# Performance work log

Hardware: AMD Instinct MI355X
Metric: run time of the kernel (lower is better)

Reference implementation:

```python
import jax, jax.numpy as jnp
import numpy as np

BN_EPS = 1e-5


def lstm_scan(x, Wih, Whh, b):
    # x: [B, T, I] -> outputs [B, T, H]; PyTorch gate order i, f, g, o
    B = x.shape[0]
    H = Whh.shape[1]
    xs = jnp.swapaxes(x, 0, 1)  # [T, B, I]

    def step(carry, xt):
        h, c = carry
        z = xt @ Wih.T + h @ Whh.T + b  # [B, 4H]
        i, f, g, o = jnp.split(z, 4, axis=-1)
        c = jax.nn.sigmoid(f) * c + jax.nn.sigmoid(i) * jnp.tanh(g)
        h = jax.nn.sigmoid(o) * jnp.tanh(c)
        return (h, c), h

    init = (jnp.zeros((B, H), x.dtype), jnp.zeros((B, H), x.dtype))
    _, hs = jax.lax.scan(step, init, xs)
    return jnp.swapaxes(hs, 0, 1)


def bilstm(x, Wf, Uf, bf, Wr, Ur, br):
    fwd = lstm_scan(x, Wf, Uf, bf)
    rev = lstm_scan(x[:, ::-1], Wr, Ur, br)[:, ::-1]
    return jnp.concatenate([fwd, rev], axis=-1)


def batchnorm(x, g, b):
    # training-mode BN: batch mean, biased variance (PyTorch forward default)
    mu = x.mean(axis=0)
    var = x.var(axis=0)
    return g * (x - mu) * jax.lax.rsqrt(var + BN_EPS) + b


def setup_inputs() -> dict:
    key = jax.random.key(0)
    ks = jax.random.split(key, 20)
    B = 1048576
    idx = jax.random.randint(ks[0], (B, 1), 0, 8).astype(jnp.float32)
    feats = jax.random.normal(ks[1], (B, 7), dtype=jnp.float32)
    x = jnp.concatenate([idx, feats], axis=1)  # [B, 8]

    def p(k, shape):
        return 0.1 * jax.random.normal(k, shape, dtype=jnp.float32)

    return {
        "x": x,
        "emb": p(ks[2], (8, 2)),
        "W1": p(ks[3], (18, 9)), "b1": p(ks[4], (18,)),
        "g1": jnp.ones((18,), jnp.float32), "be1": jnp.zeros((18,), jnp.float32),
        "W2": p(ks[5], (9, 18)), "b2": p(ks[6], (9,)),
        "g2": jnp.ones((9,), jnp.float32), "be2": jnp.zeros((9,), jnp.float32),
        # lstm1: input 1, hidden 2, bidirectional
        "l1Wf": p(ks[7], (8, 1)), "l1Uf": p(ks[8], (8, 2)), "l1bf": p(ks[9], (8,)),
        "l1Wr": p(ks[10], (8, 1)), "l1Ur": p(ks[11], (8, 2)), "l1br": p(ks[12], (8,)),
        # lstm2: input 4, hidden 1, bidirectional
        "l2Wf": p(ks[13], (4, 4)), "l2Uf": p(ks[14], (4, 1)), "l2bf": p(ks[15], (4,)),
        "l2Wr": p(ks[16], (4, 4)), "l2Ur": p(ks[17], (4, 1)), "l2br": p(ks[18], (4,)),
    }


def reference(x, emb, W1, b1, g1, be1, W2, b2, g2, be2,
              l1Wf, l1Uf, l1bf, l1Wr, l1Ur, l1br,
              l2Wf, l2Uf, l2bf, l2Wr, l2Ur, l2br):
    idx = x[:, 0].astype(jnp.int32)
    e = emb[idx]                                   # [B, 2]
    h = jnp.concatenate([e, x[:, 1:]], axis=1)     # [B, 9]
    h = jax.nn.relu(batchnorm(h @ W1.T + b1, g1, be1))   # [B, 18]
    h = jax.nn.relu(batchnorm(h @ W2.T + b2, g2, be2))   # [B, 9]
    h = h[:, :, None]                              # [B, 9, 1]
    h = jax.nn.relu(bilstm(h, l1Wf, l1Uf, l1bf, l1Wr, l1Ur, l1br))  # [B, 9, 4]
    h = bilstm(h, l2Wf, l2Uf, l2bf, l2Wr, l2Ur, l2br)               # [B, 9, 2]
    return h.reshape(-1, 9, 2)
```

## Files before the change

kernel.cpp:

```cpp
#include <hip/hip_runtime.h>

#define LOG2E 1.4426950408889634f
#define BN_EPS 1e-5f

typedef float f32x2 __attribute__((ext_vector_type(2)));
typedef float f32x4 __attribute__((ext_vector_type(4)));

__device__ __forceinline__ float sigf(float x){
    return __builtin_amdgcn_rcpf(1.f + __builtin_amdgcn_exp2f(-LOG2E * x));
}
__device__ __forceinline__ float sigtanh(float a, float b){
    float A  = __builtin_amdgcn_exp2f(LOG2E * a);
    float Bv = __builtin_amdgcn_exp2f((2.f * LOG2E) * b);
    float num = A * (Bv - 1.f);
    float den = (1.f + A) * (1.f + Bv);
    return num * __builtin_amdgcn_rcpf(den);
}
__device__ __forceinline__ float relu_(float x){ return fmaxf(x, 0.f); }

__device__ __forceinline__ float wsum(float v){
    #pragma unroll
    for (int m = 32; m >= 1; m >>= 1) v += __shfl_xor(v, m, 64);
    return v;
}

__device__ constexpr int TRI(int j, int l){ return j*9 - j*(j-1)/2 + (l - j); }

__device__ __forceinline__ void load_h0(const float* __restrict__ x, const float* __restrict__ emb,
                                        long row, float h0[9])
{
    const float4* xv = (const float4*)(x + row * 8);
    float4 p = xv[0];
    float4 q = xv[1];
    int idx = (int)p.x;
    float2 e = ((const float2*)emb)[idx];
    h0[0] = e.x; h0[1] = e.y;
    h0[2] = p.y; h0[3] = p.z; h0[4] = p.w;
    h0[5] = q.x; h0[6] = q.y; h0[7] = q.z; h0[8] = q.w;
}

__global__ __launch_bounds__(256) void k_moments(const float* __restrict__ x, const float* __restrict__ emb,
                                                 float* __restrict__ stats, int B)
{
    float s9[9], mt[45];
    #pragma unroll
    for (int j = 0; j < 9; ++j) s9[j] = 0.f;
    #pragma unroll
    for (int t = 0; t < 45; ++t) mt[t] = 0.f;

    long base = (long)blockIdx.x * 1024 + threadIdx.x;
    #pragma unroll
    for (int r = 0; r < 4; ++r){
        long row = base + r * 256;
        if (row < B){
            float h0[9];
            load_h0(x, emb, row, h0);
            #pragma unroll
            for (int j = 0; j < 9; ++j){
                s9[j] += h0[j];
                #pragma unroll
                for (int l = j; l < 9; ++l)
                    mt[TRI(j,l)] = fmaf(h0[j], h0[l], mt[TRI(j,l)]);
            }
        }
    }
    __shared__ float sm[54];
    if (threadIdx.x < 54) sm[threadIdx.x] = 0.f;
    __syncthreads();
    bool l0 = (threadIdx.x & 63) == 0;
    #pragma unroll
    for (int j = 0; j < 9; ++j){
        float v = wsum(s9[j]);
        if (l0) atomicAdd(&sm[j], v);
    }
    #pragma unroll
    for (int t = 0; t < 45; ++t){
        float v = wsum(mt[t]);
        if (l0) atomicAdd(&sm[9 + t], v);
    }
    __syncthreads();
    if (threadIdx.x < 9)  atomicAdd(&stats[threadIdx.x], sm[threadIdx.x]);
    else if (threadIdx.x < 54) atomicAdd(&stats[16 + threadIdx.x - 9], sm[threadIdx.x]);
}

__device__ __forceinline__ void bn1_from_moments(const float* __restrict__ stats,
                                                 const float* __restrict__ W1, const float* __restrict__ b1,
                                                 const float* __restrict__ g1, const float* __restrict__ be1,
                                                 float invB, float* smem_sc, float* smem_sh)
{
    if (threadIdx.x < 18){
        int k = threadIdx.x;
        float w[9];
        #pragma unroll
        for (int j = 0; j < 9; ++j) w[j] = W1[k*9 + j];
        float dot9 = 0.f, q = 0.f;
        #pragma unroll
        for (int j = 0; j < 9; ++j){
            dot9 = fmaf(w[j], stats[j], dot9);
            q = fmaf(w[j]*w[j], stats[16 + TRI(j,j)], q);
            #pragma unroll
            for (int l = j+1; l < 9; ++l)
                q = fmaf(2.f*w[j]*w[l], stats[16 + TRI(j,l)], q);
        }
        float m1  = dot9 * invB;
        float var = fmaf(-m1, m1, q * invB);
        float mu  = m1 + b1[k];
        float sc  = g1[k] * __builtin_amdgcn_rsqf(var + BN_EPS);
        smem_sc[k] = sc;
        smem_sh[k] = fmaf(-mu, sc, be1[k]);
    }
    __syncthreads();
}

template<int STORE_Z2>
__global__ __launch_bounds__(256) void k_stats2(const float* __restrict__ x, const float* __restrict__ emb,
                                                const float* __restrict__ W1, const float* __restrict__ b1,
                                                const float* __restrict__ g1, const float* __restrict__ be1,
                                                const float* __restrict__ W2, const float* __restrict__ b2,
                                                float* __restrict__ stats, float* __restrict__ z2buf, int B)
{
    __shared__ float s_sc[18], s_sh[18];
    bn1_from_moments(stats, W1, b1, g1, be1, 1.f/(float)B, s_sc, s_sh);

    float sc1[18], sh1[18];
    #pragma unroll
    for (int k = 0; k < 18; ++k){ sc1[k] = s_sc[k]; sh1[k] = s_sh[k]; }

    float as[9], aq[9];
    #pragma unroll
    for (int k = 0; k < 9; ++k){ as[k] = 0.f; aq[k] = 0.f; }

    long base = (long)blockIdx.x * 1024 + threadIdx.x;
    #pragma unroll
    for (int r = 0; r < 4; ++r){
        long row = base + r * 256;
        if (row < B){
            float h0[9];
            load_h0(x, emb, row, h0);
            float a1[18];
            #pragma unroll
            for (int k = 0; k < 18; ++k){
                float s = b1[k];
                #pragma unroll
                for (int j = 0; j < 9; ++j) s = fmaf(W1[k*9 + j], h0[j], s);
                a1[k] = relu_(fmaf(sc1[k], s, sh1[k]));
            }
            #pragma unroll
            for (int k = 0; k < 9; ++k){
                float s = b2[k];
                #pragma unroll
                for (int j = 0; j < 18; ++j) s = fmaf(W2[k*18 + j], a1[j], s);
                as[k] += s; aq[k] = fmaf(s, s, aq[k]);
                if (STORE_Z2) z2buf[(long)k * B + row] = s;
            }
        }
    }
    __shared__ float sm[18];
    if (threadIdx.x < 18) sm[threadIdx.x] = 0.f;
    __syncthreads();
    bool l0 = (threadIdx.x & 63) == 0;
    #pragma unroll
    for (int k = 0; k < 9; ++k){
        float s = wsum(as[k]);
        float q = wsum(aq[k]);
        if (l0){ atomicAdd(&sm[k], s); atomicAdd(&sm[9 + k], q); }
    }
    __syncthreads();
    if (threadIdx.x < 9)       atomicAdd(&stats[64 + threadIdx.x], sm[threadIdx.x]);
    else if (threadIdx.x < 18) atomicAdd(&stats[80 + threadIdx.x - 9], sm[threadIdx.x]);
}

__device__ __forceinline__ f32x2 mk2(float a, float b){ f32x2 r; r.x=a; r.y=b; return r; }
__device__ __forceinline__ f32x4 mk4(float a, float b, float c, float d){ f32x4 r; r.x=a; r.y=b; r.z=c; r.w=d; return r; }

template<int USE_WS>
__global__ __launch_bounds__(256) void k_main(const float* __restrict__ x, const float* __restrict__ emb,
    const float* __restrict__ W1, const float* __restrict__ b1,
    const float* __restrict__ g1, const float* __restrict__ be1,
    const float* __restrict__ W2, const float* __restrict__ b2,
    const float* __restrict__ g2, const float* __restrict__ be2,
    const float* __restrict__ w1f, const float* __restrict__ u1f, const float* __restrict__ c1f,
    const float* __restrict__ w1r, const float* __restrict__ u1r, const float* __restrict__ c1r,
    const float* __restrict__ w2f, const float* __restrict__ u2f, const float* __restrict__ c2f,
    const float* __restrict__ w2r, const float* __restrict__ u2r, const float* __restrict__ c2r,
    const float* __restrict__ stats, const float* __restrict__ z2buf,
    float* __restrict__ out, int B)
{
    __shared__ float s_sc[18], s_sh[18];
    float invB = 1.f / (float)B;
    if (!USE_WS) bn1_from_moments(stats, W1, b1, g1, be1, invB, s_sc, s_sh);

    long row = (long)blockIdx.x * 256 + threadIdx.x;
    if (row >= B) return;

    float a2[9];
    #pragma unroll
    for (int k = 0; k < 9; ++k){
        float zc;
        if (USE_WS){
            zc = z2buf[(long)k * B + row];
        } else {
            zc = 0.f;
        }
        a2[k] = zc;
    }
    if (!USE_WS){
        float h0[9];
        load_h0(x, emb, row, h0);
        float a1[18];
        #pragma unroll
        for (int k = 0; k < 18; ++k){
            float s = b1[k];
            #pragma unroll
            for (int j = 0; j < 9; ++j) s = fmaf(W1[k*9 + j], h0[j], s);
            a1[k] = relu_(fmaf(s_sc[k], s, s_sh[k]));
        }
        #pragma unroll
        for (int k = 0; k < 9; ++k){
            float s = b2[k];
            #pragma unroll
            for (int j = 0; j < 18; ++j) s = fmaf(W2[k*18 + j], a1[j], s);
            a2[k] = s;
        }
    }
    #pragma unroll
    for (int k = 0; k < 9; ++k){
        float mu  = stats[64 + k] * invB;
        float var = fmaf(-mu, mu, stats[80 + k] * invB);
        float sc  = g2[k] * __builtin_amdgcn_rsqf(var + BN_EPS);
        a2[k] = relu_(fmaf(sc, a2[k] - mu, be2[k]));
    }

    f32x4 W4[4], U04[4], U14[4], B4[4];
    #pragma unroll
    for (int g = 0; g < 4; ++g){
        W4[g]  = mk4(w1f[2*g], w1f[2*g+1], w1r[2*g], w1r[2*g+1]);
        U04[g] = mk4(u1f[(2*g)*2], u1f[(2*g+1)*2], u1r[(2*g)*2], u1r[(2*g+1)*2]);
        U14[g] = mk4(u1f[(2*g)*2+1], u1f[(2*g+1)*2+1], u1r[(2*g)*2+1], u1r[(2*g+1)*2+1]);
        B4[g]  = mk4(c1f[2*g], c1f[2*g+1], c1r[2*g], c1r[2*g+1]);
    }
    f32x4 h4 = {0.f, 0.f, 0.f, 0.f};
    f32x4 c4 = {0.f, 0.f, 0.f, 0.f};
    float u_[9][4];
    #pragma unroll
    for (int s = 0; s < 9; ++s){
        const int tf = s, tr = 8 - s;
        f32x4 xt4 = mk4(a2[tf], a2[tf], a2[tr], a2[tr]);
        f32x4 hx  = mk4(h4.x, h4.x, h4.z, h4.z);
        f32x4 hy  = mk4(h4.y, h4.y, h4.w, h4.w);
        f32x4 z[4];
        #pragma unroll
        for (int g = 0; g < 4; ++g)
            z[g] = __builtin_elementwise_fma(W4[g], xt4,
                    __builtin_elementwise_fma(U04[g], hx,
                     __builtin_elementwise_fma(U14[g], hy, B4[g])));
        f32x4 icg, fs;
        #pragma unroll
        for (int c = 0; c < 4; ++c){
            icg[c] = sigtanh(z[0][c], z[2][c]);
            fs[c]  = sigf(z[1][c]);
        }
        c4 = __builtin_elementwise_fma(fs, c4, icg);
        #pragma unroll
        for (int c = 0; c < 4; ++c) h4[c] = sigtanh(z[3][c], c4[c]);
        u_[tf][0] = relu_(h4.x);
        u_[tf][1] = relu_(h4.y);
        u_[tr][2] = relu_(h4.z);
        u_[tr][3] = relu_(h4.w);
    }

    f32x2 w2v[4][4], u2v[4], b2v[4];
    #pragma unroll
    for (int r = 0; r < 4; ++r){
        #pragma unroll
        for (int j = 0; j < 4; ++j) w2v[r][j] = mk2(w2f[4*r + j], w2r[4*r + j]);
        u2v[r] = mk2(u2f[r], u2r[r]);
        b2v[r] = mk2(c2f[r], c2r[r]);
    }
    f32x2 h2 = {0.f, 0.f};
    f32x2 cc = {0.f, 0.f};
    long obase = row * 18;
    #pragma unroll
    for (int s = 0; s < 9; ++s){
        const int tf = s, tr = 8 - s;
        f32x2 z[4];
        #pragma unroll
        for (int r = 0; r < 4; ++r){
            f32x2 acc = __builtin_elementwise_fma(u2v[r], h2, b2v[r]);
            #pragma unroll
            for (int j = 0; j < 4; ++j)
                acc = __builtin_elementwise_fma(w2v[r][j], mk2(u_[tf][j], u_[tr][j]), acc);
            z[r] = acc;
        }
        f32x2 icg, fs;
        #pragma unroll
        for (int c = 0; c < 2; ++c){
            icg[c] = sigtanh(z[0][c], z[2][c]);
            fs[c]  = sigf(z[1][c]);
        }
        cc = __builtin_elementwise_fma(fs, cc, icg);
        float hfo = sigtanh(z[3][0], cc.x);
        float hro = sigtanh(z[3][1], cc.y);
        h2 = mk2(hfo, hro);
        out[obase + 2*tf]     = hfo;
        out[obase + 2*tr + 1] = hro;
    }
}

extern "C" void kernel_launch(void* const* d_in, const int* in_sizes, int n_in,
                              void* d_out, int out_size, void* d_ws, size_t ws_size,
                              hipStream_t stream)
{
    const float* x    = (const float*)d_in[0];
    const float* emb  = (const float*)d_in[1];
    const float* W1   = (const float*)d_in[2];
    const float* b1   = (const float*)d_in[3];
    const float* g1   = (const float*)d_in[4];
    const float* be1  = (const float*)d_in[5];
    const float* W2   = (const float*)d_in[6];
    const float* b2   = (const float*)d_in[7];
    const float* g2   = (const float*)d_in[8];
    const float* be2  = (const float*)d_in[9];
    const float* l1Wf = (const float*)d_in[10];
    const float* l1Uf = (const float*)d_in[11];
    const float* l1bf = (const float*)d_in[12];
    const float* l1Wr = (const float*)d_in[13];
    const float* l1Ur = (const float*)d_in[14];
    const float* l1br = (const float*)d_in[15];
    const float* l2Wf = (const float*)d_in[16];
    const float* l2Uf = (const float*)d_in[17];
    const float* l2bf = (const float*)d_in[18];
    const float* l2Wr = (const float*)d_in[19];
    const float* l2Ur = (const float*)d_in[20];
    const float* l2br = (const float*)d_in[21];

    int B = in_sizes[0] / 8;
    float* stats = (float*)d_ws;
    float* z2buf = (float*)d_ws + 1024;
    size_t need = (1024 + (size_t)9 * B) * sizeof(float);
    bool use_ws = ws_size >= need;

    hipMemsetAsync(d_ws, 0, 128 * sizeof(float), stream);

    int nb12 = (B + 1023) / 1024;
    int nb3  = (B + 255) / 256;

    k_moments<<<nb12, 256, 0, stream>>>(x, emb, stats, B);
    if (use_ws){
        k_stats2<1><<<nb12, 256, 0, stream>>>(x, emb, W1, b1, g1, be1, W2, b2, stats, z2buf, B);
        k_main<1><<<nb3, 256, 0, stream>>>(x, emb, W1, b1, g1, be1, W2, b2, g2, be2,
                                           l1Wf, l1Uf, l1bf, l1Wr, l1Ur, l1br,
                                           l2Wf, l2Uf, l2bf, l2Wr, l2Ur, l2br,
                                           stats, z2buf, (float*)d_out, B);
    } else {
        k_stats2<0><<<nb12, 256, 0, stream>>>(x, emb, W1, b1, g1, be1, W2, b2, stats, z2buf, B);
        k_main<0><<<nb3, 256, 0, stream>>>(x, emb, W1, b1, g1, be1, W2, b2, g2, be2,
                                           l1Wf, l1Uf, l1bf, l1Wr, l1Ur, l1br,
                                           l2Wf, l2Uf, l2bf, l2Wr, l2Ur, l2br,
                                           stats, z2buf, (float*)d_out, B);
    }
}
```

Baseline: 152.9 us.

## Fuse moment and BN2 stat passes with grid barrier, add prep kernel, persistent grids

```diff
diff --git a/kernel.cpp b/kernel.cpp
--- a/kernel.cpp
+++ b/kernel.cpp
@@ -3,19 +3,15 @@
 #define LOG2E 1.4426950408889634f
 #define BN_EPS 1e-5f
 
-typedef float f32x2 __attribute__((ext_vector_type(2)));
-typedef float f32x4 __attribute__((ext_vector_type(4)));
-
-__device__ __forceinline__ float sigf(float x){
-    return __builtin_amdgcn_rcpf(1.f + __builtin_amdgcn_exp2f(-LOG2E * x));
-}
-__device__ __forceinline__ float sigtanh(float a, float b){
-    float A  = __builtin_amdgcn_exp2f(LOG2E * a);
-    float Bv = __builtin_amdgcn_exp2f((2.f * LOG2E) * b);
-    float num = A * (Bv - 1.f);
-    float den = (1.f + A) * (1.f + Bv);
-    return num * __builtin_amdgcn_rcpf(den);
-}
+#define WS_BAR   120
+#define WS_L1    128
+#define WS_L2    192
+#define WS_BN2S  240
+#define WS_BN2H  249
+#define WS_BN1S  258
+#define WS_BN1H  276
+#define WS_Z2    1024
+
 __device__ __forceinline__ float relu_(float x){ return fmaxf(x, 0.f); }
 
 __device__ __forceinline__ float wsum(float v){
@@ -25,6 +21,10 @@
 }
 
 __device__ constexpr int TRI(int j, int l){ return j*9 - j*(j-1)/2 + (l - j); }
+
+__device__ __forceinline__ float ld_stat(const float* p){
+    return __hip_atomic_load(p, __ATOMIC_RELAXED, __HIP_MEMORY_SCOPE_AGENT);
+}
 
 __device__ __forceinline__ void load_h0(const float* __restrict__ x, const float* __restrict__ emb,
                                         long row, float h0[9])
@@ -39,271 +39,327 @@
     h0[5] = q.x; h0[6] = q.y; h0[7] = q.z; h0[8] = q.w;
 }
 
-__global__ __launch_bounds__(256) void k_moments(const float* __restrict__ x, const float* __restrict__ emb,
-                                                 float* __restrict__ stats, int B)
-{
-    float s9[9], mt[45];
-    #pragma unroll
-    for (int j = 0; j < 9; ++j) s9[j] = 0.f;
-    #pragma unroll
-    for (int t = 0; t < 45; ++t) mt[t] = 0.f;
-
-    long base = (long)blockIdx.x * 1024 + threadIdx.x;
-    #pragma unroll
-    for (int r = 0; r < 4; ++r){
-        long row = base + r * 256;
-        if (row < B){
-            float h0[9];
-            load_h0(x, emb, row, h0);
-            #pragma unroll
-            for (int j = 0; j < 9; ++j){
-                s9[j] += h0[j];
-                #pragma unroll
-                for (int l = j; l < 9; ++l)
-                    mt[TRI(j,l)] = fmaf(h0[j], h0[l], mt[TRI(j,l)]);
-            }
-        }
-    }
-    __shared__ float sm[54];
-    if (threadIdx.x < 54) sm[threadIdx.x] = 0.f;
+__device__ __forceinline__ float cellh(float zi, float zfn, float zg2, float zo, float& c){
+    float A  = __builtin_amdgcn_exp2f(zi);
+    float G  = __builtin_amdgcn_exp2f(zg2);
+    float icg = A * (G - 1.f) * __builtin_amdgcn_rcpf((1.f + A) * (1.f + G));
+    float Fp = __builtin_amdgcn_exp2f(zfn);
+    float fs = __builtin_amdgcn_rcpf(1.f + Fp);
+    c = fmaf(fs, c, icg);
+    float O  = __builtin_amdgcn_exp2f(zo);
+    float T  = __builtin_amdgcn_exp2f((2.f * LOG2E) * c);
+    return O * (T - 1.f) * __builtin_amdgcn_rcpf((1.f + O) * (1.f + T));
+}
+
+struct KParams {
+    const float *x, *emb, *W1, *b1, *g1, *be1, *W2, *b2, *g2, *be2;
+    const float *w1f, *u1f, *c1f, *w1r, *u1r, *c1r;
+    const float *w2f, *u2f, *c2f, *w2r, *u2r, *c2r;
+    float* ws;
+    float* out;
+    int B;
+};
+
+__device__ __forceinline__ void gridbar(int* ctr, int nb){
     __syncthreads();
-    bool l0 = (threadIdx.x & 63) == 0;
-    #pragma unroll
-    for (int j = 0; j < 9; ++j){
-        float v = wsum(s9[j]);
-        if (l0) atomicAdd(&sm[j], v);
-    }
-    #pragma unroll
-    for (int t = 0; t < 45; ++t){
-        float v = wsum(mt[t]);
-        if (l0) atomicAdd(&sm[9 + t], v);
+    if (threadIdx.x == 0){
+        __threadfence();
+        atomicAdd(ctr, 1);
+        while (__hip_atomic_load(ctr, __ATOMIC_ACQUIRE, __HIP_MEMORY_SCOPE_AGENT) < nb)
+            __builtin_amdgcn_s_sleep(8);
     }
     __syncthreads();
-    if (threadIdx.x < 9)  atomicAdd(&stats[threadIdx.x], sm[threadIdx.x]);
-    else if (threadIdx.x < 54) atomicAdd(&stats[16 + threadIdx.x - 9], sm[threadIdx.x]);
-}
-
-__device__ __forceinline__ void bn1_from_moments(const float* __restrict__ stats,
-                                                 const float* __restrict__ W1, const float* __restrict__ b1,
-                                                 const float* __restrict__ g1, const float* __restrict__ be1,
-                                                 float invB, float* smem_sc, float* smem_sh)
+}
+
+template<int STORE_Z2>
+__global__ __launch_bounds__(256, 4) void kA(KParams p)
 {
-    if (threadIdx.x < 18){
-        int k = threadIdx.x;
+    const int tid = threadIdx.x;
+    const float invB = 1.f / (float)p.B;
+    const bool l0 = (tid & 63) == 0;
+    float* stats = p.ws;
+    const int nr = (p.B + 262143) >> 18;
+
+    {
+        float s9[9], mt[45];
+        #pragma unroll
+        for (int j = 0; j < 9; ++j) s9[j] = 0.f;
+        #pragma unroll
+        for (int t = 0; t < 45; ++t) mt[t] = 0.f;
+
+        for (int it = 0; it < nr; ++it){
+            long row = (long)it * 262144 + (long)blockIdx.x * 256 + tid;
+            if (row < p.B){
+                float h0[9];
+                load_h0(p.x, p.emb, row, h0);
+                #pragma unroll
+                for (int j = 0; j < 9; ++j){
+                    s9[j] += h0[j];
+                    #pragma unroll
+                    for (int l = j; l < 9; ++l)
+                        mt[TRI(j,l)] = fmaf(h0[j], h0[l], mt[TRI(j,l)]);
+                }
+            }
+        }
+        __shared__ float sm[54];
+        if (tid < 54) sm[tid] = 0.f;
+        __syncthreads();
+        #pragma unroll
+        for (int j = 0; j < 9; ++j){
+            float v = wsum(s9[j]);
+            if (l0) atomicAdd(&sm[j], v);
+        }
+        #pragma unroll
+        for (int t = 0; t < 45; ++t){
+            float v = wsum(mt[t]);
+            if (l0) atomicAdd(&sm[9 + t], v);
+        }
+        __syncthreads();
+        if (tid < 9)       atomicAdd(&stats[tid], sm[tid]);
+        else if (tid < 54) atomicAdd(&stats[16 + tid - 9], sm[tid]);
+    }
+
+    gridbar((int*)(stats + WS_BAR), 1024);
+
+    {
+        __shared__ float s_sc[18], s_sh[18];
+        if (tid < 18){
+            int k = tid;
+            float w[9];
+            #pragma unroll
+            for (int j = 0; j < 9; ++j) w[j] = p.W1[k*9 + j];
+            float dot9 = 0.f, q = 0.f;
+            #pragma unroll
+            for (int j = 0; j < 9; ++j){
+                dot9 = fmaf(w[j], ld_stat(&stats[j]), dot9);
+                q = fmaf(w[j]*w[j], ld_stat(&stats[16 + TRI(j,j)]), q);
+                #pragma unroll
+                for (int l = j+1; l < 9; ++l)
+                    q = fmaf(2.f*w[j]*w[l], ld_stat(&stats[16 + TRI(j,l)]), q);
+            }
+            float m1  = dot9 * invB;
+            float var = fmaf(-m1, m1, q * invB);
+            float mu  = m1 + p.b1[k];
+            float sc  = p.g1[k] * __builtin_amdgcn_rsqf(var + BN_EPS);
+            s_sc[k] = sc;
+            s_sh[k] = fmaf(-mu, sc, p.be1[k]);
+        }
+        __syncthreads();
+
+        float as[9], aq[9];
+        #pragma unroll
+        for (int k = 0; k < 9; ++k){ as[k] = 0.f; aq[k] = 0.f; }
+
+        float* z2buf = p.ws + WS_Z2;
+        for (int it = 0; it < nr; ++it){
+            long row = (long)it * 262144 + (long)blockIdx.x * 256 + tid;
+            if (row < p.B){
+                float h0[9];
+                load_h0(p.x, p.emb, row, h0);
+                float a1[18];
+                #pragma unroll
+                for (int k = 0; k < 18; ++k){
+                    float s = p.b1[k];
+                    #pragma unroll
+                    for (int j = 0; j < 9; ++j) s = fmaf(p.W1[k*9 + j], h0[j], s);
+                    a1[k] = relu_(fmaf(s_sc[k], s, s_sh[k]));
+                }
+                #pragma unroll
+                for (int k = 0; k < 9; ++k){
+                    float s = p.b2[k];
+                    #pragma unroll
+                    for (int j = 0; j < 18; ++j) s = fmaf(p.W2[k*18 + j], a1[j], s);
+                    if (STORE_Z2) z2buf[(long)k * p.B + row] = s;
+                    as[k] += s; aq[k] = fmaf(s, s, aq[k]);
+                }
+            }
+        }
+        __shared__ float sm2[18];
+        if (tid < 18) sm2[tid] = 0.f;
+        __syncthreads();
+        #pragma unroll
+        for (int k = 0; k < 9; ++k){
+            float s = wsum(as[k]);
+            float q = wsum(aq[k]);
+            if (l0){ atomicAdd(&sm2[k], s); atomicAdd(&sm2[9 + k], q); }
+        }
+        __syncthreads();
+        if (tid < 9)       atomicAdd(&stats[64 + tid], sm2[tid]);
+        else if (tid < 18) atomicAdd(&stats[80 + tid - 9], sm2[tid]);
+    }
+}
+
+__global__ void kPrep(KParams p)
+{
+    const int tid = threadIdx.x;
+    const float invB = 1.f / (float)p.B;
+    float* ws = p.ws;
+    const float scl[4] = { LOG2E, -LOG2E, 2.f*LOG2E, LOG2E };
+
+    if (tid < 18){
+        int k = tid;
         float w[9];
         #pragma unroll
-        for (int j = 0; j < 9; ++j) w[j] = W1[k*9 + j];
+        for (int j = 0; j < 9; ++j) w[j] = p.W1[k*9 + j];
         float dot9 = 0.f, q = 0.f;
         #pragma unroll
         for (int j = 0; j < 9; ++j){
-            dot9 = fmaf(w[j], stats[j], dot9);
-            q = fmaf(w[j]*w[j], stats[16 + TRI(j,j)], q);
+            dot9 = fmaf(w[j], ld_stat(&ws[j]), dot9);
+            q = fmaf(w[j]*w[j], ld_stat(&ws[16 + TRI(j,j)]), q);
             #pragma unroll
             for (int l = j+1; l < 9; ++l)
-                q = fmaf(2.f*w[j]*w[l], stats[16 + TRI(j,l)], q);
+                q = fmaf(2.f*w[j]*w[l], ld_stat(&ws[16 + TRI(j,l)]), q);
         }
         float m1  = dot9 * invB;
         float var = fmaf(-m1, m1, q * invB);
-        float mu  = m1 + b1[k];
-        float sc  = g1[k] * __builtin_amdgcn_rsqf(var + BN_EPS);
-        smem_sc[k] = sc;
-        smem_sh[k] = fmaf(-mu, sc, be1[k]);
+        float mu  = m1 + p.b1[k];
+        float sc  = p.g1[k] * __builtin_amdgcn_rsqf(var + BN_EPS);
+        ws[WS_BN1S + k] = sc;
+        ws[WS_BN1H + k] = fmaf(-mu, sc, p.be1[k]);
+    } else if (tid >= 32 && tid < 48){
+        int r = tid - 32;
+        int dir = r >> 3, rr = r & 7;
+        const float* W = dir ? p.w1r : p.w1f;
+        const float* U = dir ? p.u1r : p.u1f;
+        const float* Bb = dir ? p.c1r : p.c1f;
+        float sc = scl[rr >> 1];
+        float* dst = ws + WS_L1 + dir * 32;
+        dst[rr]            = sc * W[rr];
+        dst[8 + 2*rr]      = sc * U[2*rr];
+        dst[8 + 2*rr + 1]  = sc * U[2*rr + 1];
+        dst[24 + rr]       = sc * Bb[rr];
+    } else if (tid >= 48 && tid < 56){
+        int r = tid - 48;
+        int dir = r >> 2, rr = r & 3;
+        const float* W = dir ? p.w2r : p.w2f;
+        const float* U = dir ? p.u2r : p.u2f;
+        const float* Bb = dir ? p.c2r : p.c2f;
+        float sc = scl[rr];
+        float* dst = ws + WS_L2 + dir * 24;
+        #pragma unroll
+        for (int j = 0; j < 4; ++j) dst[4*rr + j] = sc * W[4*rr + j];
+        dst[16 + rr] = sc * U[rr];
+        dst[20 + rr] = sc * Bb[rr];
+    } else if (tid >= 64 && tid < 73){
+        int k = tid - 64;
+        float mu  = ld_stat(&ws[64 + k]) * invB;
+        float var = fmaf(-mu, mu, ld_stat(&ws[80 + k]) * invB);
+        float sc  = p.g2[k] * __builtin_amdgcn_rsqf(var + BN_EPS);
+        ws[WS_BN2S + k] = sc;
+        ws[WS_BN2H + k] = fmaf(-mu, sc, p.be2[k]);
     }
-    __syncthreads();
-}
-
-template<int STORE_Z2>
-__global__ __launch_bounds__(256) void k_stats2(const float* __restrict__ x, const float* __restrict__ emb,
-                                                const float* __restrict__ W1, const float* __restrict__ b1,
-                                                const float* __restrict__ g1, const float* __restrict__ be1,
-                                                const float* __restrict__ W2, const float* __restrict__ b2,
-                                                float* __restrict__ stats, float* __restrict__ z2buf, int B)
+}
+
+template<int USE_WS>
+__global__ __launch_bounds__(256) void kB(KParams p)
 {
-    __shared__ float s_sc[18], s_sh[18];
-    bn1_from_moments(stats, W1, b1, g1, be1, 1.f/(float)B, s_sc, s_sh);
-
-    float sc1[18], sh1[18];
-    #pragma unroll
-    for (int k = 0; k < 18; ++k){ sc1[k] = s_sc[k]; sh1[k] = s_sh[k]; }
-
-    float as[9], aq[9];
-    #pragma unroll
-    for (int k = 0; k < 9; ++k){ as[k] = 0.f; aq[k] = 0.f; }
-
-    long base = (long)blockIdx.x * 1024 + threadIdx.x;
-    #pragma unroll
-    for (int r = 0; r < 4; ++r){
-        long row = base + r * 256;
-        if (row < B){
+    const int tid = threadIdx.x;
+    const float* ws = p.ws;
+    const float* z2buf = ws + WS_Z2;
+    const float* L1F = ws + WS_L1;
+    const float* L1R = ws + WS_L1 + 32;
+    const float* L2F = ws + WS_L2;
+    const float* L2R = ws + WS_L2 + 24;
+    const int nr = (p.B + 262143) >> 18;
+
+    for (int it = 0; it < nr; ++it){
+        long row = (long)it * 262144 + (long)blockIdx.x * 256 + tid;
+        if (row >= p.B) continue;
+
+        float a2[9];
+        if (USE_WS){
+            #pragma unroll
+            for (int k = 0; k < 9; ++k){
+                float z = z2buf[(long)k * p.B + row];
+                a2[k] = relu_(fmaf(ws[WS_BN2S + k], z, ws[WS_BN2H + k]));
+            }
+        } else {
             float h0[9];
-            load_h0(x, emb, row, h0);
+            load_h0(p.x, p.emb, row, h0);
             float a1[18];
             #pragma unroll
             for (int k = 0; k < 18; ++k){
-                float s = b1[k];
-                #pragma unroll
-                for (int j = 0; j < 9; ++j) s = fmaf(W1[k*9 + j], h0[j], s);
-                a1[k] = relu_(fmaf(sc1[k], s, sh1[k]));
+                float s = p.b1[k];
+                #pragma unroll
+                for (int j = 0; j < 9; ++j) s = fmaf(p.W1[k*9 + j], h0[j], s);
+                a1[k] = relu_(fmaf(ws[WS_BN1S + k], s, ws[WS_BN1H + k]));
             }
             #pragma unroll
             for (int k = 0; k < 9; ++k){
-                float s = b2[k];
-                #pragma unroll
-                for (int j = 0; j < 18; ++j) s = fmaf(W2[k*18 + j], a1[j], s);
-                as[k] += s; aq[k] = fmaf(s, s, aq[k]);
-                if (STORE_Z2) z2buf[(long)k * B + row] = s;
-            }
-        }
-    }
-    __shared__ float sm[18];
-    if (threadIdx.x < 18) sm[threadIdx.x] = 0.f;
-    __syncthreads();
-    bool l0 = (threadIdx.x & 63) == 0;
-    #pragma unroll
-    for (int k = 0; k < 9; ++k){
-        float s = wsum(as[k]);
-        float q = wsum(aq[k]);
-        if (l0){ atomicAdd(&sm[k], s); atomicAdd(&sm[9 + k], q); }
-    }
-    __syncthreads();
-    if (threadIdx.x < 9)       atomicAdd(&stats[64 + threadIdx.x], sm[threadIdx.x]);
-    else if (threadIdx.x < 18) atomicAdd(&stats[80 + threadIdx.x - 9], sm[threadIdx.x]);
-}
-
-__device__ __forceinline__ f32x2 mk2(float a, float b){ f32x2 r; r.x=a; r.y=b; return r; }
-__device__ __forceinline__ f32x4 mk4(float a, float b, float c, float d){ f32x4 r; r.x=a; r.y=b; r.z=c; r.w=d; return r; }
-
-template<int USE_WS>
-__global__ __launch_bounds__(256) void k_main(const float* __restrict__ x, const float* __restrict__ emb,
-    const float* __restrict__ W1, const float* __restrict__ b1,
-    const float* __restrict__ g1, const float* __restrict__ be1,
-    const float* __restrict__ W2, const float* __restrict__ b2,
-    const float* __restrict__ g2, const float* __restrict__ be2,
-    const float* __restrict__ w1f, const float* __restrict__ u1f, const float* __restrict__ c1f,
-    const float* __restrict__ w1r, const float* __restrict__ u1r, const float* __restrict__ c1r,
-    const float* __restrict__ w2f, const float* __restrict__ u2f, const float* __restrict__ c2f,
-    const float* __restrict__ w2r, const float* __restrict__ u2r, const float* __restrict__ c2r,
-    const float* __restrict__ stats, const float* __restrict__ z2buf,
-    float* __restrict__ out, int B)
-{
-    __shared__ float s_sc[18], s_sh[18];
-    float invB = 1.f / (float)B;
-    if (!USE_WS) bn1_from_moments(stats, W1, b1, g1, be1, invB, s_sc, s_sh);
-
-    long row = (long)blockIdx.x * 256 + threadIdx.x;
-    if (row >= B) return;
-
-    float a2[9];
-    #pragma unroll
-    for (int k = 0; k < 9; ++k){
-        float zc;
-        if (USE_WS){
-            zc = z2buf[(long)k * B + row];
-        } else {
-            zc = 0.f;
-        }
-        a2[k] = zc;
-    }
-    if (!USE_WS){
-        float h0[9];
-        load_h0(x, emb, row, h0);
-        float a1[18];
-        #pragma unroll
-        for (int k = 0; k < 18; ++k){
-            float s = b1[k];
-            #pragma unroll
-            for (int j = 0; j < 9; ++j) s = fmaf(W1[k*9 + j], h0[j], s);
-            a1[k] = relu_(fmaf(s_sc[k], s, s_sh[k]));
-        }
-        #pragma unroll
-        for (int k = 0; k < 9; ++k){
-            float s = b2[k];
-            #pragma unroll
-            for (int j = 0; j < 18; ++j) s = fmaf(W2[k*18 + j], a1[j], s);
-            a2[k] = s;
-        }
-    }
-    #pragma unroll
-    for (int k = 0; k < 9; ++k){
-        float mu  = stats[64 + k] * invB;
-        float var = fmaf(-mu, mu, stats[80 + k] * invB);
-        float sc  = g2[k] * __builtin_amdgcn_rsqf(var + BN_EPS);
-        a2[k] = relu_(fmaf(sc, a2[k] - mu, be2[k]));
-    }
-
-    f32x4 W4[4], U04[4], U14[4], B4[4];
-    #pragma unroll
-    for (int g = 0; g < 4; ++g){
-        W4[g]  = mk4(w1f[2*g], w1f[2*g+1], w1r[2*g], w1r[2*g+1]);
-        U04[g] = mk4(u1f[(2*g)*2], u1f[(2*g+1)*2], u1r[(2*g)*2], u1r[(2*g+1)*2]);
-        U14[g] = mk4(u1f[(2*g)*2+1], u1f[(2*g+1)*2+1], u1r[(2*g)*2+1], u1r[(2*g+1)*2+1]);
-        B4[g]  = mk4(c1f[2*g], c1f[2*g+1], c1r[2*g], c1r[2*g+1]);
-    }
-    f32x4 h4 = {0.f, 0.f, 0.f, 0.f};
-    f32x4 c4 = {0.f, 0.f, 0.f, 0.f};
-    float u_[9][4];
-    #pragma unroll
-    for (int s = 0; s < 9; ++s){
-        const int tf = s, tr = 8 - s;
-        f32x4 xt4 = mk4(a2[tf], a2[tf], a2[tr], a2[tr]);
-        f32x4 hx  = mk4(h4.x, h4.x, h4.z, h4.z);
-        f32x4 hy  = mk4(h4.y, h4.y, h4.w, h4.w);
-        f32x4 z[4];
-        #pragma unroll
-        for (int g = 0; g < 4; ++g)
-            z[g] = __builtin_elementwise_fma(W4[g], xt4,
-                    __builtin_elementwise_fma(U04[g], hx,
-                     __builtin_elementwise_fma(U14[g], hy, B4[g])));
-        f32x4 icg, fs;
-        #pragma unroll
-        for (int c = 0; c < 4; ++c){
-            icg[c] = sigtanh(z[0][c], z[2][c]);
-            fs[c]  = sigf(z[1][c]);
-        }
-        c4 = __builtin_elementwise_fma(fs, c4, icg);
-        #pragma unroll
-        for (int c = 0; c < 4; ++c) h4[c] = sigtanh(z[3][c], c4[c]);
-        u_[tf][0] = relu_(h4.x);
-        u_[tf][1] = relu_(h4.y);
-        u_[tr][2] = relu_(h4.z);
-        u_[tr][3] = relu_(h4.w);
-    }
-
-    f32x2 w2v[4][4], u2v[4], b2v[4];
-    #pragma unroll
-    for (int r = 0; r < 4; ++r){
-        #pragma unroll
-        for (int j = 0; j < 4; ++j) w2v[r][j] = mk2(w2f[4*r + j], w2r[4*r + j]);
-        u2v[r] = mk2(u2f[r], u2r[r]);
-        b2v[r] = mk2(c2f[r], c2r[r]);
-    }
-    f32x2 h2 = {0.f, 0.f};
-    f32x2 cc = {0.f, 0.f};
-    long obase = row * 18;
-    #pragma unroll
-    for (int s = 0; s < 9; ++s){
-        const int tf = s, tr = 8 - s;
-        f32x2 z[4];
-        #pragma unroll
-        for (int r = 0; r < 4; ++r){
-            f32x2 acc = __builtin_elementwise_fma(u2v[r], h2, b2v[r]);
-            #pragma unroll
-            for (int j = 0; j < 4; ++j)
-                acc = __builtin_elementwise_fma(w2v[r][j], mk2(u_[tf][j], u_[tr][j]), acc);
-            z[r] = acc;
-        }
-        f32x2 icg, fs;
-        #pragma unroll
-        for (int c = 0; c < 2; ++c){
-            icg[c] = sigtanh(z[0][c], z[2][c]);
-            fs[c]  = sigf(z[1][c]);
-        }
-        cc = __builtin_elementwise_fma(fs, cc, icg);
-        float hfo = sigtanh(z[3][0], cc.x);
-        float hro = sigtanh(z[3][1], cc.y);
-        h2 = mk2(hfo, hro);
-        out[obase + 2*tf]     = hfo;
-        out[obase + 2*tr + 1] = hro;
+                float s = p.b2[k];
+                #pragma unroll
+                for (int j = 0; j < 18; ++j) s = fmaf(p.W2[k*18 + j], a1[j], s);
+                a2[k] = relu_(fmaf(ws[WS_BN2S + k], s, ws[WS_BN2H + k]));
+            }
+        }
+
+        float hf0 = 0.f, hf1 = 0.f, cf0 = 0.f, cf1 = 0.f;
+        float hr0 = 0.f, hr1 = 0.f, cr0 = 0.f, cr1 = 0.f;
+        float u_[9][4];
+        #pragma unroll
+        for (int s = 0; s < 9; ++s){
+            const int tf = s, tr = 8 - s;
+            float xf = a2[tf], xr = a2[tr];
+            {
+                const float* W = L1F; const float* U = L1F + 8; const float* Bb = L1F + 24;
+                float zi0 = fmaf(W[0], xf, fmaf(U[0],  hf0, fmaf(U[1],  hf1, Bb[0])));
+                float zi1 = fmaf(W[1], xf, fmaf(U[2],  hf0, fmaf(U[3],  hf1, Bb[1])));
+                float zf0 = fmaf(W[2], xf, fmaf(U[4],  hf0, fmaf(U[5],  hf1, Bb[2])));
+                float zf1 = fmaf(W[3], xf, fmaf(U[6],  hf0, fmaf(U[7],  hf1, Bb[3])));
+                float zg0 = fmaf(W[4], xf, fmaf(U[8],  hf0, fmaf(U[9],  hf1, Bb[4])));
+                float zg1 = fmaf(W[5], xf, fmaf(U[10], hf0, fmaf(U[11], hf1, Bb[5])));
+                float zo0 = fmaf(W[6], xf, fmaf(U[12], hf0, fmaf(U[13], hf1, Bb[6])));
+                float zo1 = fmaf(W[7], xf, fmaf(U[14], hf0, fmaf(U[15], hf1, Bb[7])));
+                hf0 = cellh(zi0, zf0, zg0, zo0, cf0);
+                hf1 = cellh(zi1, zf1, zg1, zo1, cf1);
+            }
+            {
+                const float* W = L1R; const float* U = L1R + 8; const float* Bb = L1R + 24;
+                float zi0 = fmaf(W[0], xr, fmaf(U[0],  hr0, fmaf(U[1],  hr1, Bb[0])));
+                float zi1 = fmaf(W[1], xr, fmaf(U[2],  hr0, fmaf(U[3],  hr1, Bb[1])));
+                float zf0 = fmaf(W[2], xr, fmaf(U[4],  hr0, fmaf(U[5],  hr1, Bb[2])));
+                float zf1 = fmaf(W[3], xr, fmaf(U[6],  hr0, fmaf(U[7],  hr1, Bb[3])));
+                float zg0 = fmaf(W[4], xr, fmaf(U[8],  hr0, fmaf(U[9],  hr1, Bb[4])));
+                float zg1 = fmaf(W[5], xr, fmaf(U[10], hr0, fmaf(U[11], hr1, Bb[5])));
+                float zo0 = fmaf(W[6], xr, fmaf(U[12], hr0, fmaf(U[13], hr1, Bb[6])));
+                float zo1 = fmaf(W[7], xr, fmaf(U[14], hr0, fmaf(U[15], hr1, Bb[7])));
+                hr0 = cellh(zi0, zf0, zg0, zo0, cr0);
+                hr1 = cellh(zi1, zf1, zg1, zo1, cr1);
+            }
+            u_[tf][0] = relu_(hf0);
+            u_[tf][1] = relu_(hf1);
+            u_[tr][2] = relu_(hr0);
+            u_[tr][3] = relu_(hr1);
+        }
+
+        float h2f = 0.f, c2f = 0.f, h2r = 0.f, c2r = 0.f;
+        float of[9], orr[9];
+        #pragma unroll
+        for (int s = 0; s < 9; ++s){
+            const int tf = s, tr = 8 - s;
+            {
+                const float* W = L2F; const float* U = L2F + 16; const float* Bb = L2F + 20;
+                float zi = fmaf(W[0],  u_[tf][0], fmaf(W[1],  u_[tf][1], fmaf(W[2],  u_[tf][2], fmaf(W[3],  u_[tf][3], fmaf(U[0], h2f, Bb[0])))));
+                float zf = fmaf(W[4],  u_[tf][0], fmaf(W[5],  u_[tf][1], fmaf(W[6],  u_[tf][2], fmaf(W[7],  u_[tf][3], fmaf(U[1], h2f, Bb[1])))));
+                float zg = fmaf(W[8],  u_[tf][0], fmaf(W[9],  u_[tf][1], fmaf(W[10], u_[tf][2], fmaf(W[11], u_[tf][3], fmaf(U[2], h2f, Bb[2])))));
+                float zo = fmaf(W[12], u_[tf][0], fmaf(W[13], u_[tf][1], fmaf(W[14], u_[tf][2], fmaf(W[15], u_[tf][3], fmaf(U[3], h2f, Bb[3])))));
+                h2f = cellh(zi, zf, zg, zo, c2f);
+                of[tf] = h2f;
+            }
+            {
+                const float* W = L2R; const float* U = L2R + 16; const float* Bb = L2R + 20;
+                float zi = fmaf(W[0],  u_[tr][0], fmaf(W[1],  u_[tr][1], fmaf(W[2],  u_[tr][2], fmaf(W[3],  u_[tr][3], fmaf(U[0], h2r, Bb[0])))));
+                float zf = fmaf(W[4],  u_[tr][0], fmaf(W[5],  u_[tr][1], fmaf(W[6],  u_[tr][2], fmaf(W[7],  u_[tr][3], fmaf(U[1], h2r, Bb[1])))));
+                float zg = fmaf(W[8],  u_[tr][0], fmaf(W[9],  u_[tr][1], fmaf(W[10], u_[tr][2], fmaf(W[11], u_[tr][3], fmaf(U[2], h2r, Bb[2])))));
+                float zo = fmaf(W[12], u_[tr][0], fmaf(W[13], u_[tr][1], fmaf(W[14], u_[tr][2], fmaf(W[15], u_[tr][3], fmaf(U[3], h2r, Bb[3])))));
+                h2r = cellh(zi, zf, zg, zo, c2r);
+                orr[tr] = h2r;
+            }
+        }
+
+        float2* op = (float2*)(p.out + row * 18);
+        #pragma unroll
+        for (int t = 0; t < 9; ++t) op[t] = make_float2(of[t], orr[t]);
     }
 }
 
@@ -311,52 +367,42 @@
                               void* d_out, int out_size, void* d_ws, size_t ws_size,
                               hipStream_t stream)
 {
-    const float* x    = (const float*)d_in[0];
-    const float* emb  = (const float*)d_in[1];
-    const float* W1   = (const float*)d_in[2];
-    const float* b1   = (const float*)d_in[3];
-    const float* g1   = (const float*)d_in[4];
-    const float* be1  = (const float*)d_in[5];
-    const float* W2   = (const float*)d_in[6];
-    const float* b2   = (const float*)d_in[7];
-    const float* g2   = (const float*)d_in[8];
-    const float* be2  = (const float*)d_in[9];
-    const float* l1Wf = (const float*)d_in[10];
-    const float* l1Uf = (const float*)d_in[11];
-    const float* l1bf = (const float*)d_in[12];
-    const float* l1Wr = (const float*)d_in[13];
-    const float* l1Ur = (const float*)d_in[14];
-    const float* l1br = (const float*)d_in[15];
-    const float* l2Wf = (const float*)d_in[16];
-    const float* l2Uf = (const float*)d_in[17];
-    const float* l2bf = (const float*)d_in[18];
-    const float* l2Wr = (const float*)d_in[19];
-    const float* l2Ur = (const float*)d_in[20];
-    const float* l2br = (const float*)d_in[21];
-
-    int B = in_sizes[0] / 8;
-    float* stats = (float*)d_ws;
-    float* z2buf = (float*)d_ws + 1024;
-    size_t need = (1024 + (size_t)9 * B) * sizeof(float);
-    bool use_ws = ws_size >= need;
-
-    hipMemsetAsync(d_ws, 0, 128 * sizeof(float), stream);
-
-    int nb12 = (B + 1023) / 1024;
-    int nb3  = (B + 255) / 256;
-
-    k_moments<<<nb12, 256, 0, stream>>>(x, emb, stats, B);
-    if (use_ws){
-        k_stats2<1><<<nb12, 256, 0, stream>>>(x, emb, W1, b1, g1, be1, W2, b2, stats, z2buf, B);
-        k_main<1><<<nb3, 256, 0, stream>>>(x, emb, W1, b1, g1, be1, W2, b2, g2, be2,
-                                           l1Wf, l1Uf, l1bf, l1Wr, l1Ur, l1br,
-                                           l2Wf, l2Uf, l2bf, l2Wr, l2Ur, l2br,
-                                           stats, z2buf, (float*)d_out, B);
-    } else {
-        k_stats2<0><<<nb12, 256, 0, stream>>>(x, emb, W1, b1, g1, be1, W2, b2, stats, z2buf, B);
-        k_main<0><<<nb3, 256, 0, stream>>>(x, emb, W1, b1, g1, be1, W2, b2, g2, be2,
-                                           l1Wf, l1Uf, l1bf, l1Wr, l1Ur, l1br,
-                                           l2Wf, l2Uf, l2bf, l2Wr, l2Ur, l2br,
-                                           stats, z2buf, (float*)d_out, B);
-    }
-}
+    KParams p;
+    p.x    = (const float*)d_in[0];
+    p.emb  = (const float*)d_in[1];
+    p.W1   = (const float*)d_in[2];
+    p.b1   = (const float*)d_in[3];
+    p.g1   = (const float*)d_in[4];
+    p.be1  = (const float*)d_in[5];
+    p.W2   = (const float*)d_in[6];
+    p.b2   = (const float*)d_in[7];
+    p.g2   = (const float*)d_in[8];
+    p.be2  = (const float*)d_in[9];
+    p.w1f  = (const float*)d_in[10];
+    p.u1f  = (const float*)d_in[11];
+    p.c1f  = (const float*)d_in[12];
+    p.w1r  = (const float*)d_in[13];
+    p.u1r  = (const float*)d_in[14];
+    p.c1r  = (const float*)d_in[15];
+    p.w2f  = (const float*)d_in[16];
+    p.u2f  = (const float*)d_in[17];
+    p.c2f  = (const float*)d_in[18];
+    p.w2r  = (const float*)d_in[19];
+    p.u2r  = (const float*)d_in[20];
+    p.c2r  = (const float*)d_in[21];
+    p.ws   = (float*)d_ws;
+    p.out  = (float*)d_out;
+    p.B    = in_sizes[0] / 8;
+
+    bool use_ws = ws_size >= (size_t)(WS_Z2 + 9 * (size_t)p.B) * sizeof(float);
+
+    hipMemsetAsync(d_ws, 0, 512, stream);
+
+    if (use_ws) kA<1><<<1024, 256, 0, stream>>>(p);
+    else        kA<0><<<1024, 256, 0, stream>>>(p);
+
+    kPrep<<<1, 128, 0, stream>>>(p);
+
+    if (use_ws) kB<1><<<1024, 256, 0, stream>>>(p);
+    else        kB<0><<<1024, 256, 0, stream>>>(p);
+}
```

New measurement: 265.1 us. +73.3%, slower.
